# Kernel tuning notes

Hardware: AMD Instinct MI355X
Metric: run time of the kernel (lower is better)

## Reference

```python
import jax, jax.numpy as jnp
import numpy as np

NEG_SLOPE = 0.2
EPS = 1e-16
HEADS1, OUT1 = 4, 32
HEADS2, OUT2 = 1, 32


def _gat_conv(x, W, a_src, a_dst, bias, src, dst, num_nodes, heads, out_c, concat):
    # x: [N, F_in], W: [F_in, heads*out_c], a_*: [heads, out_c]
    h = (x @ W).reshape(num_nodes, heads, out_c)            # [N, H, C]
    alpha_src = (h * a_src).sum(-1)                          # [N, H]
    alpha_dst = (h * a_dst).sum(-1)                          # [N, H]
    e = jax.nn.leaky_relu(alpha_src[src] + alpha_dst[dst], NEG_SLOPE)  # [E, H]
    # softmax over incoming edges of each destination node (PyG softmax)
    m = jax.ops.segment_max(e, dst, num_segments=num_nodes)
    ex = jnp.exp(e - m[dst])
    s = jax.ops.segment_sum(ex, dst, num_segments=num_nodes)
    alpha = ex / (s[dst] + EPS)                              # [E, H]
    out = jax.ops.segment_sum(h[src] * alpha[:, :, None], dst,
                              num_segments=num_nodes)        # [N, H, C]
    out = out.reshape(num_nodes, heads * out_c) if concat else out.mean(axis=1)
    return out + bias


def setup_inputs() -> dict:
    key = jax.random.key(0)
    ks = jax.random.split(key, 10)
    N, E, F_IN = 50000, 1600000, 128
    sc = 0.1
    return {
        "x": jax.random.normal(ks[0], (N, F_IN), jnp.float32),
        "edge_index": jax.random.randint(ks[1], (2, E), 0, N, jnp.int32),
        "W1": jax.random.normal(ks[2], (F_IN, HEADS1 * OUT1), jnp.float32) * sc,
        "a_src1": jax.random.normal(ks[3], (HEADS1, OUT1), jnp.float32) * sc,
        "a_dst1": jax.random.normal(ks[4], (HEADS1, OUT1), jnp.float32) * sc,
        "b1": jax.random.normal(ks[5], (HEADS1 * OUT1,), jnp.float32) * sc,
        "W2": jax.random.normal(ks[6], (HEADS1 * OUT1, HEADS2 * OUT2), jnp.float32) * sc,
        "a_src2": jax.random.normal(ks[7], (HEADS2, OUT2), jnp.float32) * sc,
        "a_dst2": jax.random.normal(ks[8], (HEADS2, OUT2), jnp.float32) * sc,
        "b2": jax.random.normal(ks[9], (OUT2,), jnp.float32) * sc,
    }


def reference(x, edge_index, W1, a_src1, a_dst1, b1, W2, a_src2, a_dst2, b2):
    N = x.shape[0]
    # PyG GATConv default add_self_loops=True
    loops = jnp.arange(N, dtype=edge_index.dtype)
    src = jnp.concatenate([edge_index[0], loops])
    dst = jnp.concatenate([edge_index[1], loops])
    h = _gat_conv(x, W1, a_src1, a_dst1, b1, src, dst, N, HEADS1, OUT1, True)
    h = jax.nn.elu(h)
    return _gat_conv(h, W2, a_src2, a_dst2, b2, src, dst, N, HEADS2, OUT2, False)
```

## Files before the change

kernel.cpp:

```cpp
#include <hip/hip_runtime.h>
#include <math.h>

#define NEG_SLOPE 0.2f
#define EPSV 1e-16f
#define NPART 16

typedef _Float16 half4 __attribute__((ext_vector_type(4)));
typedef _Float16 half8 __attribute__((ext_vector_type(8)));


__global__ void k_scan_blk(const int* __restrict__ degp, int N,
                           int* __restrict__ rowptr, int* __restrict__ bsum){
    int b = blockIdx.x, t = threadIdx.x;
    int base = b * 1024 + t * 4;
    int v[4];
    #pragma unroll
    for (int j = 0; j < 4; j++){
        int n = base + j, s = 0;
        if (n < N){
            #pragma unroll
            for (int p = 0; p < NPART; p++) s += degp[p * N + n];
        }
        v[j] = s;
    }
    int s = v[0] + v[1] + v[2] + v[3];
    int lane = t & 63, wid = t >> 6;
    int x = s;
    #pragma unroll
    for (int off = 1; off < 64; off <<= 1){
        int y = __shfl_up(x, off, 64);
        if (lane >= off) x += y;
    }
    __shared__ int ws[4];
    if (lane == 63) ws[wid] = x;
    __syncthreads();
    int woff = 0;
    for (int w = 0; w < wid; w++) woff += ws[w];
    int run = woff + x - s;
    #pragma unroll
    for (int j = 0; j < 4; j++){
        if (base + j < N) rowptr[base + j] = run;
        run += v[j];
    }
    if (t == 255) bsum[b] = woff + x;
}

__global__ void k_finalize(const int* __restrict__ bsum, const int* __restrict__ degp,
                           int N, int ET,
                           int* __restrict__ rowptr, int* __restrict__ poff){
    int b = blockIdx.x, t = threadIdx.x;
    int n = b * 256 + t;
    int chunk = (b * 256) >> 10;
    int off = 0;
    for (int c = 0; c < chunk; c++) off += bsum[c];
    if (n < N){
        int r = rowptr[n] + off;
        rowptr[n] = r;
        int run = r;
        #pragma unroll
        for (int p = 0; p < NPART; p++){
            poff[p * N + n] = run;
            run += degp[p * N + n];
        }
    }
    if (n == 0) rowptr[N] = ET;
}

__launch_bounds__(256)
__global__ void k_scatter2(const int* __restrict__ ei, int E, int ET, int N,
                           const int* __restrict__ poff,
                           const unsigned short* __restrict__ rank,
                           int* __restrict__ csr_src){
    int i = blockIdx.x * 256 + threadIdx.x;
    if (i >= ET) return;
    int s, d;
    if (i < E){ s = ei[i]; d = ei[E + i]; } else { s = i - E; d = s; }
    int p = (i >> 8) & (NPART - 1);
    csr_src[poff[p * N + d] + (int)rank[i]] = s;
}


__launch_bounds__(256)
__global__ void k_gemm1_hist(const float* __restrict__ x, const float* __restrict__ W1,
                             const float* __restrict__ a_src, const float* __restrict__ a_dst,
                             _Float16* __restrict__ h1h, float* __restrict__ asrc1,
                             float* __restrict__ adst1, int N, int nGemmBlk,
                             const int* __restrict__ ei, int E, int ET,
                             int* __restrict__ degp, unsigned short* __restrict__ rank){
    __shared__ float Wl[32 * 128];
    __shared__ float xl[32 * 128];
    int t = threadIdx.x;
    if ((int)blockIdx.x >= nGemmBlk){
        int base = (blockIdx.x - nGemmBlk) * 512 + t;
        #pragma unroll
        for (int j = 0; j < 2; j++){
            int i = base + j * 256;
            if (i < ET){
                int d = (i < E) ? ei[E + i] : (i - E);
                int p = (i >> 8) & (NPART - 1);
                rank[i] = (unsigned short)atomicAdd(&degp[p * N + d], 1);
            }
        }
        return;
    }
    int cg = t & 31, ns = t >> 5;
    int n0 = blockIdx.x * 32;
    for (int idx = t; idx < 1024; idx += 256){
        int row = idx >> 5, k4 = idx & 31;
        float4 v = {0.f, 0.f, 0.f, 0.f};
        if (n0 + row < N) v = *(const float4*)&x[(size_t)(n0 + row) * 128 + k4 * 4];
        *(float4*)&xl[row * 128 + k4 * 4] = v;
    }
    float4 acc0 = {0,0,0,0}, acc1 = {0,0,0,0}, acc2 = {0,0,0,0}, acc3 = {0,0,0,0};
    for (int c = 0; c < 4; c++){
        __syncthreads();
        for (int idx = t; idx < 1024; idx += 256)
            *(float4*)&Wl[idx * 4] = *(const float4*)&W1[c * 32 * 128 + idx * 4];
        __syncthreads();
        #pragma unroll 2
        for (int k = 0; k < 32; k += 4){
            float4 xv0 = *(float4*)&xl[(ns     ) * 128 + c * 32 + k];
            float4 xv1 = *(float4*)&xl[(ns +  8) * 128 + c * 32 + k];
            float4 xv2 = *(float4*)&xl[(ns + 16) * 128 + c * 32 + k];
            float4 xv3 = *(float4*)&xl[(ns + 24) * 128 + c * 32 + k];
            #pragma unroll
            for (int kk = 0; kk < 4; kk++){
                float4 w = *(float4*)&Wl[(k + kk) * 128 + cg * 4];
                float x0 = ((float*)&xv0)[kk];
                float x1 = ((float*)&xv1)[kk];
                float x2v= ((float*)&xv2)[kk];
                float x3 = ((float*)&xv3)[kk];
                acc0.x = fmaf(x0, w.x, acc0.x); acc0.y = fmaf(x0, w.y, acc0.y);
                acc0.z = fmaf(x0, w.z, acc0.z); acc0.w = fmaf(x0, w.w, acc0.w);
                acc1.x = fmaf(x1, w.x, acc1.x); acc1.y = fmaf(x1, w.y, acc1.y);
                acc1.z = fmaf(x1, w.z, acc1.z); acc1.w = fmaf(x1, w.w, acc1.w);
                acc2.x = fmaf(x2v, w.x, acc2.x); acc2.y = fmaf(x2v, w.y, acc2.y);
                acc2.z = fmaf(x2v, w.z, acc2.z); acc2.w = fmaf(x2v, w.w, acc2.w);
                acc3.x = fmaf(x3, w.x, acc3.x); acc3.y = fmaf(x3, w.y, acc3.y);
                acc3.z = fmaf(x3, w.z, acc3.z); acc3.w = fmaf(x3, w.w, acc3.w);
            }
        }
    }
    float4 a4s = *(const float4*)&a_src[cg * 4];
    float4 a4d = *(const float4*)&a_dst[cg * 4];
    float4 accs[4] = {acc0, acc1, acc2, acc3};
    #pragma unroll
    for (int j = 0; j < 4; j++){
        int n = n0 + ns + 8 * j;
        if (n >= N) continue;
        float4 a = accs[j];
        half4 hv;
        hv.x = (_Float16)a.x; hv.y = (_Float16)a.y;
        hv.z = (_Float16)a.z; hv.w = (_Float16)a.w;
        *(half4*)&h1h[((size_t)n << 7) + (cg << 2)] = hv;
        float vs = a.x * a4s.x + a.y * a4s.y + a.z * a4s.z + a.w * a4s.w;
        float vd = a.x * a4d.x + a.y * a4d.y + a.z * a4d.z + a.w * a4d.w;
        #pragma unroll
        for (int m = 1; m <= 4; m <<= 1){
            vs += __shfl_xor(vs, m, 64);
            vd += __shfl_xor(vd, m, 64);
        }
        if ((cg & 7) == 0){
            int head = cg >> 3;
            asrc1[n * 4 + head] = vs;
            adst1[n * 4 + head] = vd;
        }
    }
}


__launch_bounds__(256)
__global__ void k_agg1(const int* __restrict__ rowptr, const int* __restrict__ csr_src,
                       const float* __restrict__ asrc1, const float* __restrict__ adst1,
                       const _Float16* __restrict__ h1h,
                       const float* __restrict__ b1, float* __restrict__ x2){
    int t = threadIdx.x;
    int n = blockIdx.x * 4 + (t >> 6);
    int lane = t & 63, g = lane >> 4, l = lane & 15, head = l >> 2;
    int start = rowptr[n], end = rowptr[n + 1];
    float adn = adst1[(n << 2) + head];
    const char* hb = (const char*)h1h;
    const char* ab = (const char*)asrc1;
    int hoff = l << 4;
    int aoff = head << 2;
    float rA[8] = {0,0,0,0,0,0,0,0}, rB[8] = {0,0,0,0,0,0,0,0};
    float sA = 0.f, sB = 0.f;
    int i = start + g;
    for (; i + 4 < end; i += 8){
        int s0 = csr_src[i];
        int s1 = csr_src[i + 4];
        float e0 = *(const float*)(ab + (s0 << 4) + aoff) + adn;
        float e1 = *(const float*)(ab + (s1 << 4) + aoff) + adn;
        e0 = fmaxf(e0, NEG_SLOPE * e0);
        e1 = fmaxf(e1, NEG_SLOPE * e1);
        float w0 = __expf(e0);
        float w1 = __expf(e1);
        half8 h0 = *(const half8*)(hb + (s0 << 8) + hoff);
        half8 h1v = *(const half8*)(hb + (s1 << 8) + hoff);
        sA += w0; sB += w1;
        #pragma unroll
        for (int j = 0; j < 8; j++){
            rA[j] = fmaf(w0, (float)h0[j], rA[j]);
            rB[j] = fmaf(w1, (float)h1v[j], rB[j]);
        }
    }
    if (i < end){
        int s0 = csr_src[i];
        float e0 = *(const float*)(ab + (s0 << 4) + aoff) + adn;
        e0 = fmaxf(e0, NEG_SLOPE * e0);
        float w0 = __expf(e0);
        half8 h0 = *(const half8*)(hb + (s0 << 8) + hoff);
        sA += w0;
        #pragma unroll
        for (int j = 0; j < 8; j++) rA[j] = fmaf(w0, (float)h0[j], rA[j]);
    }
    float r[9];
    #pragma unroll
    for (int j = 0; j < 8; j++) r[j] = rA[j] + rB[j];
    r[8] = sA + sB;
    #pragma unroll
    for (int m = 16; m <= 32; m <<= 1)
        #pragma unroll
        for (int j = 0; j < 9; j++) r[j] += __shfl_xor(r[j], m, 64);
    if (g == 0){
        float inv = 1.f / (r[8] + EPSV);
        float o[8];
        #pragma unroll
        for (int j = 0; j < 8; j++){
            float v = r[j] * inv + b1[l * 8 + j];
            o[j] = (v > 0.f) ? v : expm1f(v);
        }
        float4 o0 = {o[0], o[1], o[2], o[3]};
        float4 o1 = {o[4], o[5], o[6], o[7]};
        *(float4*)&x2[((size_t)n << 7) + (l << 3)]     = o0;
        *(float4*)&x2[((size_t)n << 7) + (l << 3) + 4] = o1;
    }
}


__launch_bounds__(256)
__global__ void k_gemm2(const float* __restrict__ x2, const float* __restrict__ W2,
                        const float* __restrict__ a_src, const float* __restrict__ a_dst,
                        _Float16* __restrict__ h2h, float* __restrict__ asrc2,
                        float* __restrict__ adst2, int N){
    __shared__ float Wl[128 * 32];
    __shared__ float xl[128 * 128];
    int t = threadIdx.x;
    int cg = t & 7, ns = t >> 3;
    for (int idx = t; idx < 1024; idx += 256)
        *(float4*)&Wl[idx * 4] = *(const float4*)&W2[idx * 4];
    int n0 = blockIdx.x * 128;
    for (int idx = t; idx < 4096; idx += 256){
        int row = idx >> 5, k4 = idx & 31;
        float4 v = {0.f, 0.f, 0.f, 0.f};
        if (n0 + row < N) v = *(const float4*)&x2[(size_t)(n0 + row) * 128 + k4 * 4];
        *(float4*)&xl[row * 128 + k4 * 4] = v;
    }
    __syncthreads();
    float4 acc0 = {0,0,0,0}, acc1 = {0,0,0,0}, acc2 = {0,0,0,0}, acc3 = {0,0,0,0};
    #pragma unroll 2
    for (int k = 0; k < 128; k += 4){
        float4 xv0 = *(float4*)&xl[(ns      ) * 128 + k];
        float4 xv1 = *(float4*)&xl[(ns +  32) * 128 + k];
        float4 xv2 = *(float4*)&xl[(ns +  64) * 128 + k];
        float4 xv3 = *(float4*)&xl[(ns +  96) * 128 + k];
        #pragma unroll
        for (int kk = 0; kk < 4; kk++){
            float4 w = *(float4*)&Wl[(k + kk) * 32 + cg * 4];
            float x0 = ((float*)&xv0)[kk];
            float x1 = ((float*)&xv1)[kk];
            float x2v= ((float*)&xv2)[kk];
            float x3 = ((float*)&xv3)[kk];
            acc0.x = fmaf(x0, w.x, acc0.x); acc0.y = fmaf(x0, w.y, acc0.y);
            acc0.z = fmaf(x0, w.z, acc0.z); acc0.w = fmaf(x0, w.w, acc0.w);
            acc1.x = fmaf(x1, w.x, acc1.x); acc1.y = fmaf(x1, w.y, acc1.y);
            acc1.z = fmaf(x1, w.z, acc1.z); acc1.w = fmaf(x1, w.w, acc1.w);
            acc2.x = fmaf(x2v, w.x, acc2.x); acc2.y = fmaf(x2v, w.y, acc2.y);
            acc2.z = fmaf(x2v, w.z, acc2.z); acc2.w = fmaf(x2v, w.w, acc2.w);
            acc3.x = fmaf(x3, w.x, acc3.x); acc3.y = fmaf(x3, w.y, acc3.y);
            acc3.z = fmaf(x3, w.z, acc3.z); acc3.w = fmaf(x3, w.w, acc3.w);
        }
    }
    float4 a4s = *(const float4*)&a_src[cg * 4];
    float4 a4d = *(const float4*)&a_dst[cg * 4];
    float4 accs[4] = {acc0, acc1, acc2, acc3};
    #pragma unroll
    for (int j = 0; j < 4; j++){
        int n = n0 + ns + 32 * j;
        if (n >= N) continue;
        float4 a = accs[j];
        half4 hv;
        hv.x = (_Float16)a.x; hv.y = (_Float16)a.y;
        hv.z = (_Float16)a.z; hv.w = (_Float16)a.w;
        *(half4*)&h2h[((size_t)n << 5) + (cg << 2)] = hv;
        float vs = a.x * a4s.x + a.y * a4s.y + a.z * a4s.z + a.w * a4s.w;
        float vd = a.x * a4d.x + a.y * a4d.y + a.z * a4d.z + a.w * a4d.w;
        #pragma unroll
        for (int m = 1; m <= 4; m <<= 1){
            vs += __shfl_xor(vs, m, 64);
            vd += __shfl_xor(vd, m, 64);
        }
        if (cg == 0){ asrc2[n] = vs; adst2[n] = vd; }
    }
}


__launch_bounds__(256)
__global__ void k_agg2(const int* __restrict__ rowptr, const int* __restrict__ csr_src,
                       const float* __restrict__ asrc2, const float* __restrict__ adst2,
                       const _Float16* __restrict__ h2h,
                       const float* __restrict__ b2, float* __restrict__ out){
    int t = threadIdx.x;
    int n = blockIdx.x * 4 + (t >> 6);
    int lane = t & 63, g = lane >> 3, l = lane & 7;
    int start = rowptr[n], end = rowptr[n + 1];
    float adn = adst2[n];
    const char* hb = (const char*)h2h;
    const char* ab = (const char*)asrc2;
    int hoff = l << 3;
    float4 aA = {0,0,0,0}, aB = {0,0,0,0};
    float sA = 0.f, sB = 0.f;
    int i = start + g;
    for (; i + 8 < end; i += 16){
        int s0 = csr_src[i];
        int s1 = csr_src[i + 8];
        float e0 = *(const float*)(ab + (s0 << 2)) + adn;
        float e1 = *(const float*)(ab + (s1 << 2)) + adn;
        e0 = fmaxf(e0, NEG_SLOPE * e0);
        e1 = fmaxf(e1, NEG_SLOPE * e1);
        float w0 = __expf(e0);
        float w1 = __expf(e1);
        half4 h0 = *(const half4*)(hb + (s0 << 6) + hoff);
        half4 h1v = *(const half4*)(hb + (s1 << 6) + hoff);
        sA += w0; sB += w1;
        aA.x = fmaf(w0, (float)h0.x, aA.x); aA.y = fmaf(w0, (float)h0.y, aA.y);
        aA.z = fmaf(w0, (float)h0.z, aA.z); aA.w = fmaf(w0, (float)h0.w, aA.w);
        aB.x = fmaf(w1, (float)h1v.x, aB.x); aB.y = fmaf(w1, (float)h1v.y, aB.y);
        aB.z = fmaf(w1, (float)h1v.z, aB.z); aB.w = fmaf(w1, (float)h1v.w, aB.w);
    }
    if (i < end){
        int s0 = csr_src[i];
        float e0 = *(const float*)(ab + (s0 << 2)) + adn;
        e0 = fmaxf(e0, NEG_SLOPE * e0);
        float w0 = __expf(e0);
        half4 h0 = *(const half4*)(hb + (s0 << 6) + hoff);
        sA += w0;
        aA.x = fmaf(w0, (float)h0.x, aA.x); aA.y = fmaf(w0, (float)h0.y, aA.y);
        aA.z = fmaf(w0, (float)h0.z, aA.z); aA.w = fmaf(w0, (float)h0.w, aA.w);
    }
    float4 acc = {aA.x + aB.x, aA.y + aB.y, aA.z + aB.z, aA.w + aB.w};
    float ssum = sA + sB;
    #pragma unroll
    for (int m = 8; m <= 32; m <<= 1){
        acc.x += __shfl_xor(acc.x, m, 64);
        acc.y += __shfl_xor(acc.y, m, 64);
        acc.z += __shfl_xor(acc.z, m, 64);
        acc.w += __shfl_xor(acc.w, m, 64);
        ssum  += __shfl_xor(ssum,  m, 64);
    }
    if (g == 0){
        float inv = 1.f / (ssum + EPSV);
        const float4 b4 = *(const float4*)&b2[l * 4];
        float4 o;
        o.x = acc.x * inv + b4.x; o.y = acc.y * inv + b4.y;
        o.z = acc.z * inv + b4.z; o.w = acc.w * inv + b4.w;
        *(float4*)&out[((size_t)n << 5) + l * 4] = o;
    }
}


extern "C" void kernel_launch(void* const* d_in, const int* in_sizes, int n_in,
                              void* d_out, int out_size, void* d_ws, size_t ws_size,
                              hipStream_t stream){
    const float* x      = (const float*)d_in[0];
    const int*   ei     = (const int*)  d_in[1];
    const float* W1     = (const float*)d_in[2];
    const float* a_src1 = (const float*)d_in[3];
    const float* a_dst1 = (const float*)d_in[4];
    const float* b1     = (const float*)d_in[5];
    const float* W2     = (const float*)d_in[6];
    const float* a_src2 = (const float*)d_in[7];
    const float* a_dst2 = (const float*)d_in[8];
    const float* b2     = (const float*)d_in[9];
    float* out = (float*)d_out;

    int N  = in_sizes[0] / 128;
    int E  = in_sizes[1] / 2;
    int ET = E + N;
    int nScanBlk = (N + 1023) / 1024;
    int G  = (ET + 255) / 256;
    int GH = (ET + 511) / 512;
    int nGemmBlk = (N + 31) / 32;

    char* ws = (char*)d_ws;
    size_t off = 0;
    auto alloc = [&](size_t bytes) -> char* {
        char* p = ws + off;
        off += (bytes + 255) & ~(size_t)255;
        return p;
    };
    int*            degp    = (int*)           alloc((size_t)NPART * N * 4);
    int*            rowptr  = (int*)           alloc((size_t)(N + 1) * 4);
    int*            bsum    = (int*)           alloc((size_t)nScanBlk * 4);
    unsigned short* rank    = (unsigned short*)alloc((size_t)ET * 2);
    int*            poff    = (int*)           alloc((size_t)NPART * N * 4);
    int*            csr_src = (int*)           alloc((size_t)ET * 4);
    _Float16*       h1h     = (_Float16*)      alloc((size_t)N * 128 * 2);
    float*          x2      = (float*)         alloc((size_t)N * 128 * 4);
    float*          asrc1   = (float*)         alloc((size_t)N * 4 * 4);
    float*          adst1   = (float*)         alloc((size_t)N * 4 * 4);
    _Float16*       h2h     = (_Float16*)      alloc((size_t)N * 32 * 2);
    float*          asrc2   = (float*)         alloc((size_t)N * 4);
    float*          adst2   = (float*)         alloc((size_t)N * 4);

    hipMemsetAsync(degp, 0, (size_t)NPART * N * 4, stream);
    hipLaunchKernelGGL(k_gemm1_hist, dim3(nGemmBlk + GH), dim3(256), 0, stream,
                       x, W1, a_src1, a_dst1, h1h, asrc1, adst1, N, nGemmBlk,
                       ei, E, ET, degp, rank);
    hipLaunchKernelGGL(k_scan_blk,  dim3(nScanBlk), dim3(256), 0, stream, degp, N, rowptr, bsum);
    hipLaunchKernelGGL(k_finalize,  dim3((N + 255) / 256), dim3(256), 0, stream, bsum, degp, N, ET, rowptr, poff);
    hipLaunchKernelGGL(k_scatter2,  dim3(G), dim3(256), 0, stream, ei, E, ET, N, poff, rank, csr_src);
    hipLaunchKernelGGL(k_agg1,      dim3(N / 4), dim3(256), 0, stream, rowptr, csr_src, asrc1, adst1, h1h, b1, x2);
    hipLaunchKernelGGL(k_gemm2,     dim3((N + 127) / 128), dim3(256), 0, stream, x2, W2, a_src2, a_dst2, h2h, asrc2, adst2, N);
    hipLaunchKernelGGL(k_agg2,      dim3(N / 4), dim3(256), 0, stream, rowptr, csr_src, asrc2, adst2, h2h, b2, out);
}
```

Baseline: 315.1 us.

## Shrink GEMM1 W tile, widen histogram blocks, use packed float2 FMAs in aggregation

The GEMM1 kernel now stages W1 in 16-row chunks instead of 32, cutting shared memory per block (possibly for occupancy) at the cost of twice as many barrier rounds. The histogram part of the fused kernel processes 4 edges per thread instead of 2, halving the number of histogram blocks. Both aggregation kernels rewrite their weighted accumulation with float2 vector types so the compiler can emit packed FMA instructions. These are several independent tweaks; the packed math depends on the compiler actually producing v_pk_fma_f32.

```diff
diff --git a/kernel.cpp b/kernel.cpp
--- a/kernel.cpp
+++ b/kernel.cpp
@@ -7,6 +7,7 @@
 
 typedef _Float16 half4 __attribute__((ext_vector_type(4)));
 typedef _Float16 half8 __attribute__((ext_vector_type(8)));
+typedef float floatx2 __attribute__((ext_vector_type(2)));
 
 
 __global__ void k_scan_blk(const int* __restrict__ degp, int N,
@@ -87,13 +88,13 @@
                              float* __restrict__ adst1, int N, int nGemmBlk,
                              const int* __restrict__ ei, int E, int ET,
                              int* __restrict__ degp, unsigned short* __restrict__ rank){
-    __shared__ float Wl[32 * 128];
+    __shared__ float Wl[16 * 128];
     __shared__ float xl[32 * 128];
     int t = threadIdx.x;
     if ((int)blockIdx.x >= nGemmBlk){
-        int base = (blockIdx.x - nGemmBlk) * 512 + t;
-        #pragma unroll
-        for (int j = 0; j < 2; j++){
+        int base = (blockIdx.x - nGemmBlk) * 1024 + t;
+        #pragma unroll
+        for (int j = 0; j < 4; j++){
             int i = base + j * 256;
             if (i < ET){
                 int d = (i < E) ? ei[E + i] : (i - E);
@@ -112,17 +113,17 @@
         *(float4*)&xl[row * 128 + k4 * 4] = v;
     }
     float4 acc0 = {0,0,0,0}, acc1 = {0,0,0,0}, acc2 = {0,0,0,0}, acc3 = {0,0,0,0};
-    for (int c = 0; c < 4; c++){
+    for (int c = 0; c < 8; c++){
         __syncthreads();
-        for (int idx = t; idx < 1024; idx += 256)
-            *(float4*)&Wl[idx * 4] = *(const float4*)&W1[c * 32 * 128 + idx * 4];
+        for (int idx = t; idx < 512; idx += 256)
+            *(float4*)&Wl[idx * 4] = *(const float4*)&W1[c * 16 * 128 + idx * 4];
         __syncthreads();
-        #pragma unroll 2
-        for (int k = 0; k < 32; k += 4){
-            float4 xv0 = *(float4*)&xl[(ns     ) * 128 + c * 32 + k];
-            float4 xv1 = *(float4*)&xl[(ns +  8) * 128 + c * 32 + k];
-            float4 xv2 = *(float4*)&xl[(ns + 16) * 128 + c * 32 + k];
-            float4 xv3 = *(float4*)&xl[(ns + 24) * 128 + c * 32 + k];
+        #pragma unroll
+        for (int k = 0; k < 16; k += 4){
+            float4 xv0 = *(float4*)&xl[(ns     ) * 128 + c * 16 + k];
+            float4 xv1 = *(float4*)&xl[(ns +  8) * 128 + c * 16 + k];
+            float4 xv2 = *(float4*)&xl[(ns + 16) * 128 + c * 16 + k];
+            float4 xv3 = *(float4*)&xl[(ns + 24) * 128 + c * 16 + k];
             #pragma unroll
             for (int kk = 0; kk < 4; kk++){
                 float4 w = *(float4*)&Wl[(k + kk) * 128 + cg * 4];
@@ -183,7 +184,9 @@
     const char* ab = (const char*)asrc1;
     int hoff = l << 4;
     int aoff = head << 2;
-    float rA[8] = {0,0,0,0,0,0,0,0}, rB[8] = {0,0,0,0,0,0,0,0};
+    floatx2 rA[4], rB[4];
+    #pragma unroll
+    for (int j = 0; j < 4; j++){ rA[j] = (floatx2)0.f; rB[j] = (floatx2)0.f; }
     float sA = 0.f, sB = 0.f;
     int i = start + g;
     for (; i + 4 < end; i += 8){
@@ -198,10 +201,13 @@
         half8 h0 = *(const half8*)(hb + (s0 << 8) + hoff);
         half8 h1v = *(const half8*)(hb + (s1 << 8) + hoff);
         sA += w0; sB += w1;
-        #pragma unroll
-        for (int j = 0; j < 8; j++){
-            rA[j] = fmaf(w0, (float)h0[j], rA[j]);
-            rB[j] = fmaf(w1, (float)h1v[j], rB[j]);
+        floatx2 w02 = {w0, w0}, w12 = {w1, w1};
+        #pragma unroll
+        for (int j = 0; j < 4; j++){
+            floatx2 c0 = {(float)h0[2*j], (float)h0[2*j+1]};
+            floatx2 c1 = {(float)h1v[2*j], (float)h1v[2*j+1]};
+            rA[j] = w02 * c0 + rA[j];
+            rB[j] = w12 * c1 + rB[j];
         }
     }
     if (i < end){
@@ -211,12 +217,19 @@
         float w0 = __expf(e0);
         half8 h0 = *(const half8*)(hb + (s0 << 8) + hoff);
         sA += w0;
-        #pragma unroll
-        for (int j = 0; j < 8; j++) rA[j] = fmaf(w0, (float)h0[j], rA[j]);
+        floatx2 w02 = {w0, w0};
+        #pragma unroll
+        for (int j = 0; j < 4; j++){
+            floatx2 c0 = {(float)h0[2*j], (float)h0[2*j+1]};
+            rA[j] = w02 * c0 + rA[j];
+        }
     }
     float r[9];
     #pragma unroll
-    for (int j = 0; j < 8; j++) r[j] = rA[j] + rB[j];
+    for (int j = 0; j < 4; j++){
+        floatx2 c = rA[j] + rB[j];
+        r[2*j] = c.x; r[2*j+1] = c.y;
+    }
     r[8] = sA + sB;
     #pragma unroll
     for (int m = 16; m <= 32; m <<= 1)
@@ -318,7 +331,9 @@
     const char* hb = (const char*)h2h;
     const char* ab = (const char*)asrc2;
     int hoff = l << 3;
-    float4 aA = {0,0,0,0}, aB = {0,0,0,0};
+    floatx2 aA[2], aB[2];
+    aA[0] = (floatx2)0.f; aA[1] = (floatx2)0.f;
+    aB[0] = (floatx2)0.f; aB[1] = (floatx2)0.f;
     float sA = 0.f, sB = 0.f;
     int i = start + g;
     for (; i + 8 < end; i += 16){
@@ -333,10 +348,11 @@
         half4 h0 = *(const half4*)(hb + (s0 << 6) + hoff);
         half4 h1v = *(const half4*)(hb + (s1 << 6) + hoff);
         sA += w0; sB += w1;
-        aA.x = fmaf(w0, (float)h0.x, aA.x); aA.y = fmaf(w0, (float)h0.y, aA.y);
-        aA.z = fmaf(w0, (float)h0.z, aA.z); aA.w = fmaf(w0, (float)h0.w, aA.w);
-        aB.x = fmaf(w1, (float)h1v.x, aB.x); aB.y = fmaf(w1, (float)h1v.y, aB.y);
-        aB.z = fmaf(w1, (float)h1v.z, aB.z); aB.w = fmaf(w1, (float)h1v.w, aB.w);
+        floatx2 w02 = {w0, w0}, w12 = {w1, w1};
+        floatx2 c00 = {(float)h0.x, (float)h0.y}, c01 = {(float)h0.z, (float)h0.w};
+        floatx2 c10 = {(float)h1v.x, (float)h1v.y}, c11 = {(float)h1v.z, (float)h1v.w};
+        aA[0] = w02 * c00 + aA[0]; aA[1] = w02 * c01 + aA[1];
+        aB[0] = w12 * c10 + aB[0]; aB[1] = w12 * c11 + aB[1];
     }
     if (i < end){
         int s0 = csr_src[i];
@@ -345,10 +361,12 @@
         float w0 = __expf(e0);
         half4 h0 = *(const half4*)(hb + (s0 << 6) + hoff);
         sA += w0;
-        aA.x = fmaf(w0, (float)h0.x, aA.x); aA.y = fmaf(w0, (float)h0.y, aA.y);
-        aA.z = fmaf(w0, (float)h0.z, aA.z); aA.w = fmaf(w0, (float)h0.w, aA.w);
-    }
-    float4 acc = {aA.x + aB.x, aA.y + aB.y, aA.z + aB.z, aA.w + aB.w};
+        floatx2 w02 = {w0, w0};
+        floatx2 c00 = {(float)h0.x, (float)h0.y}, c01 = {(float)h0.z, (float)h0.w};
+        aA[0] = w02 * c00 + aA[0]; aA[1] = w02 * c01 + aA[1];
+    }
+    floatx2 m0 = aA[0] + aB[0], m1 = aA[1] + aB[1];
+    float4 acc = {m0.x, m0.y, m1.x, m1.y};
     float ssum = sA + sB;
     #pragma unroll
     for (int m = 8; m <= 32; m <<= 1){
@@ -389,7 +407,7 @@
     int ET = E + N;
     int nScanBlk = (N + 1023) / 1024;
     int G  = (ET + 255) / 256;
-    int GH = (ET + 511) / 512;
+    int GH = (ET + 1023) / 1024;
     int nGemmBlk = (N + 31) / 32;
 
     char* ws = (char*)d_ws;
```

Result: no change. 316.4 us (+0.4%).
